# Kernel optimization log

Hardware: AMD Instinct MI355X
Metric: run time of the kernel (lower is better)

## Reference

```python
import jax, jax.numpy as jnp
import numpy as np

GRID_SIZE = 5
SPLINE_ORDER = 3
NUM_BASIS = GRID_SIZE + SPLINE_ORDER  # 8
BN_EPS = 1e-5


def make_grid():
    # efficient_kan extended uniform grid on [-1, 1]
    h = 2.0 / GRID_SIZE
    return (jnp.arange(-SPLINE_ORDER, GRID_SIZE + SPLINE_ORDER + 1, dtype=jnp.float32) * h) - 1.0


def b_splines(x, grid):
    """Cox-de Boor B-spline bases. x: (...,) -> (..., NUM_BASIS)."""
    x = x[..., None]
    bases = ((x >= grid[:-1]) & (x < grid[1:])).astype(x.dtype)
    for p in range(1, SPLINE_ORDER + 1):
        left = (x - grid[: -(p + 1)]) / (grid[p:-1] - grid[: -(p + 1)])
        right = (grid[p + 1:] - x) / (grid[p + 1:] - grid[1:-p])
        bases = left * bases[..., :-1] + right * bases[..., 1:]
    return bases


def grouped_conv(x, w, groups, padding):
    return jax.lax.conv_general_dilated(
        x, w, window_strides=(1, 1), padding=[(padding, padding)] * 2,
        feature_group_count=groups,
        dimension_numbers=("NCHW", "OIHW", "NCHW"))


def kan_conv(x, w_base, b_base, w_spline, grid, groups, padding):
    # base branch: grouped conv on SiLU(x)
    base = grouped_conv(jax.nn.silu(x), w_base, groups, padding)
    base = base + b_base[None, :, None, None]
    # spline branch: per-channel B-spline basis expansion (C -> C*NUM_BASIS)
    B, C, H, W = x.shape
    sp = b_splines(jnp.moveaxis(x, 1, -1), grid)            # (B,H,W,C,NB)
    sp = jnp.moveaxis(sp.reshape(B, H, W, C * NUM_BASIS), -1, 1)  # (B,C*NB,H,W)
    return base + grouped_conv(sp, w_spline, groups, padding)


def setup_inputs() -> dict:
    key = jax.random.key(0)
    ks = jax.random.split(key, 8)
    B, C_in, C_out, G, H, W = 16, 128, 256, 8, 64, 64
    x = jax.random.normal(ks[0], (B, C_in, H, W), dtype=jnp.float32)
    w_base1 = jax.random.normal(ks[1], (C_out, C_in // G, 1, 1), jnp.float32) * 0.1
    b_base1 = jnp.zeros((C_out,), jnp.float32)
    w_spline1 = jax.random.normal(ks[2], (C_out, (C_in * NUM_BASIS) // G, 1, 1), jnp.float32) * 0.05
    w_base2 = jax.random.normal(ks[3], (C_out, C_out // G, 3, 3), jnp.float32) * 0.05
    b_base2 = jnp.zeros((C_out,), jnp.float32)
    w_spline2 = jax.random.normal(ks[4], (C_out, (C_out * NUM_BASIS) // G, 3, 3), jnp.float32) * 0.02
    gamma = jnp.ones((C_out,), jnp.float32)
    beta = jnp.zeros((C_out,), jnp.float32)
    return {"x": x, "w_base1": w_base1, "b_base1": b_base1, "w_spline1": w_spline1,
            "w_base2": w_base2, "b_base2": b_base2, "w_spline2": w_spline2,
            "gamma": gamma, "beta": beta}


def reference(x, w_base1, b_base1, w_spline1, w_base2, b_base2, w_spline2, gamma, beta):
    G = 8
    grid = make_grid()
    h = kan_conv(x, w_base1, b_base1, w_spline1, grid, G, padding=0)   # 1x1 grouped KAN conv
    h = kan_conv(h, w_base2, b_base2, w_spline2, grid, G, padding=1)   # 3x3 grouped KAN conv
    # BatchNorm2d (training mode: batch statistics over N,H,W)
    mean = jnp.mean(h, axis=(0, 2, 3), keepdims=True)
    var = jnp.var(h, axis=(0, 2, 3), keepdims=True)
    hn = (h - mean) * jax.lax.rsqrt(var + BN_EPS)
    return hn * gamma[None, :, None, None] + beta[None, :, None, None]
```

## Files before the change

kernel.cpp:

```cpp
#include <hip/hip_runtime.h>
#include <hip/hip_bf16.h>
#include <stdint.h>


#define NB 8
#define NF 9
#define CIN 128
#define COUT 256
#define GROUPS 8
#define HW 4096
#define BATCH 16

#define WFS_ELEMS 589824
#define WFB_ELEMS 73728
#define WF1S_ELEMS 32768
#define WF1B_ELEMS 8192

typedef __attribute__((ext_vector_type(8))) short bf16x8;
typedef __attribute__((ext_vector_type(4))) float f32x4;

__device__ __forceinline__ unsigned bf16r(float f) {
    union { float f; unsigned u; } c; c.f = f;
    unsigned r = c.u + 0x7FFF + ((c.u >> 16) & 1);
    return r >> 16;
}
__device__ __forceinline__ unsigned bfpack2(float lo, float hi) {
    unsigned r;
    asm("v_cvt_pk_bf16_f32 %0, %1, %2" : "=v"(r) : "v"(lo), "v"(hi));
    return r;
}
__device__ __forceinline__ unsigned bfpack2_typed(float lo, float hi) {
    __hip_bfloat16 a = __float2bfloat16(lo);
    __hip_bfloat16 b = __float2bfloat16(hi);
    unsigned short ua, ub;
    __builtin_memcpy(&ua, &a, 2);
    __builtin_memcpy(&ub, &b, 2);
    return (unsigned)ua | ((unsigned)ub << 16);
}

__device__ __forceinline__ float silu_fast(float v) {
    float e = __builtin_amdgcn_exp2f(v * -1.44269504088896f);
    return v * __builtin_amdgcn_rcpf(1.0f + e);
}

__device__ __forceinline__ void spline_w(float v, float& w0, float& w1,
                                         float& w2, float& w3, int& k) {
    float s = (v + 2.2f) * 2.5f;
    float fk = floorf(s);
    k = (int)fk;
    float u = s - fk;
    float um = 1.0f - u;
    float u2 = u * u, u3 = u2 * u;
    w0 = um * um * um * (1.0f / 6.0f);
    w1 = (3.0f * u3 - 6.0f * u2 + 4.0f) * (1.0f / 6.0f);
    w2 = (-3.0f * u3 + 3.0f * u2 + 3.0f * u + 1.0f) * (1.0f / 6.0f);
    w3 = u3 * (1.0f / 6.0f);
}

__device__ __forceinline__ uint4 spline_row(float v, bool in, float& sv) {
    sv = silu_fast(v);
    float w0, w1, w2, w3; int k;
    spline_w(v, w0, w1, w2, w3, k);
    unsigned W0 = bfpack2(w0, w1);
    unsigned W1 = bfpack2(w2, w3);
    int kk = in ? (k - 3) : 99;
    unsigned odd = (unsigned)kk & 1u;
    unsigned A = W0 << 16;
    unsigned B = (W0 >> 16) | (W1 << 16);
    unsigned C = W1 >> 16;
    unsigned t0 = odd ? A : W0;
    unsigned t1 = odd ? B : W1;
    unsigned t2 = odd ? C : 0u;
    int q = kk >> 1;
    uint4 pk;
    pk.x = (q == 0) ? t0 : (q == -1) ? t1 : (q == -2) ? t2 : 0u;
    pk.y = (q == 1) ? t0 : (q == 0)  ? t1 : (q == -1) ? t2 : 0u;
    pk.z = (q == 2) ? t0 : (q == 1)  ? t1 : (q == 0)  ? t2 : 0u;
    pk.w = (q == 3) ? t0 : (q == 2)  ? t1 : (q == 1)  ? t2 : 0u;
    return pk;
}

__device__ __forceinline__ void expand_u(int raw, bool in,
                                         uint4& pk, unsigned& su) {
    float v = __uint_as_float(((unsigned)raw) << 16);
    float sv;
    pk = spline_row(v, in, sv);
    su = bf16r(sv);
}

__global__ void __launch_bounds__(256) repack2_kernel(
    const float* __restrict__ wb1, const float* __restrict__ ws1,
    const float* __restrict__ wb2, const float* __restrict__ ws2,
    unsigned short* __restrict__ wfs, unsigned short* __restrict__ wfb,
    unsigned short* __restrict__ wf1s, unsigned short* __restrict__ wf1b) {
    int i = blockIdx.x * 256 + threadIdx.x;
    if (i < WF1S_ELEMS) {
        int j = i & 7;
        int lane = (i >> 3) & 63;
        int nf = (i >> 9) & 1;
        int cc = (i >> 10) & 3;
        int g = i >> 12;
        int c_loc = cc * 4 + (lane >> 4);
        int cog = g * 32 + nf * 16 + (lane & 15);
        wf1s[i] = (unsigned short)bf16r(ws1[cog * 128 + c_loc * 8 + j]);
    }
    if (i < WF1B_ELEMS) {
        int j = i & 7;
        int lane = (i >> 3) & 63;
        int nf = (i >> 9) & 1;
        int g = (i >> 10) & 7;
        int k = (lane >> 4) * 8 + j;
        int cog = g * 32 + nf * 16 + (lane & 15);
        wf1b[i] = (k < 16) ? (unsigned short)bf16r(wb1[cog * 16 + k]) : 0;
    }
    if (i < WFB_ELEMS) {
        int j = i & 7;
        int lane = (i >> 3) & 63;
        int nf = (i >> 9) & 1;
        int t = i >> 10;
        int dy = t % 3; t /= 3;
        int dx = t % 3; t /= 3;
        int g = t;
        int ch = (lane >> 4) * 8 + j;
        int cog = g * 32 + nf * 16 + (lane & 15);
        wfb[i] = (unsigned short)bf16r(wb2[((cog * 32 + ch) * 3 + dy) * 3 + dx]);
    }
    if (i < WFS_ELEMS) {
        int j = i & 7;
        int t = i >> 3;
        int lane = t & 63; t >>= 6;
        int nf = t & 1; t >>= 1;
        int dy = t % 3; t /= 3;
        int dx = t % 3; t /= 3;
        int cc = t & 7; t >>= 3;
        int g = t;
        int c_loc = cc * 4 + (lane >> 4);
        int cog = g * 32 + nf * 16 + (lane & 15);
        float v = ws2[((cog * 256 + c_loc * 8 + j) * 3 + dy) * 3 + dx];
        wfs[i] = (unsigned short)bf16r(v);
    }
}

__global__ void __launch_bounds__(256, 4) kan1m_kernel(
    const float* __restrict__ x, const bf16x8* __restrict__ wf1s,
    const bf16x8* __restrict__ wf1b, const float* __restrict__ bb1,
    unsigned short* __restrict__ h1) {
    __shared__ __align__(16) unsigned char lds[32768];
    unsigned char* spl = lds;
    unsigned char* slu = lds + 16384;

    const int tid = threadIdx.x;
    const int lane = tid & 63;
    const int w = tid >> 6;
    const int blk = blockIdx.x;
    const int tile = blk & 15;
    const int g = (blk >> 4) & 7;
    const int b = blk >> 7;
    const int lrow = lane & 15;
    const int lhi = lane >> 4;
    const int posg0 = tile * 256;

    {
        int key = (tid >> 1) & 3;
        uint4 z = {0, 0, 0, 0};
        *reinterpret_cast<uint4*>(slu + tid * 64 + ((2 ^ key) << 4)) = z;
        *reinterpret_cast<uint4*>(slu + tid * 64 + ((3 ^ key) << 4)) = z;
    }

    const float* xg = x + ((size_t)b * CIN + g * 16) * HW + posg0;

    float xreg[4];
#pragma unroll
    for (int it = 0; it < 4; ++it) xreg[it] = xg[it * HW + tid];

    f32x4 acc[4][2];
#pragma unroll
    for (int m = 0; m < 4; ++m)
#pragma unroll
        for (int nf = 0; nf < 2; ++nf) {
            float bias = bb1[g * 32 + nf * 16 + lrow];
            acc[m][nf] = (f32x4){bias, bias, bias, bias};
        }

    for (int cc = 0; cc < 4; ++cc) {
        __syncthreads();
        int key = (tid >> 1) & 3;
#pragma unroll
        for (int it = 0; it < 4; ++it) {
            float sv;
            uint4 pk = spline_row(xreg[it], true, sv);
            *reinterpret_cast<uint4*>(spl + tid * 64 + ((it ^ key) << 4)) = pk;
            int cg = cc * 4 + it;
            *reinterpret_cast<unsigned short*>(
                slu + tid * 64 + (((cg >> 3) ^ key) << 4) + (cg & 7) * 2) =
                (unsigned short)bf16r(sv);
        }
        if (cc < 3) {
#pragma unroll
            for (int it = 0; it < 4; ++it)
                xreg[it] = xg[((cc + 1) * 4 + it) * HW + tid];
        }
        __syncthreads();
        const bf16x8* wpc = wf1s + (size_t)((g * 4 + cc) * 2) * 64;
        bf16x8 bf0 = wpc[lane];
        bf16x8 bf1 = wpc[64 + lane];
#pragma unroll
        for (int m = 0; m < 4; ++m) {
            int pos = w * 64 + m * 16 + lrow;
            int ra = pos * 64 + ((lhi ^ ((pos >> 1) & 3)) << 4);
            bf16x8 af = *reinterpret_cast<const bf16x8*>(spl + ra);
            acc[m][0] = __builtin_amdgcn_mfma_f32_16x16x32_bf16(af, bf0, acc[m][0], 0, 0, 0);
            acc[m][1] = __builtin_amdgcn_mfma_f32_16x16x32_bf16(af, bf1, acc[m][1], 0, 0, 0);
        }
    }
    {
        const bf16x8* wpb = wf1b + (size_t)(g * 2) * 64;
        bf16x8 bf0 = wpb[lane];
        bf16x8 bf1 = wpb[64 + lane];
#pragma unroll
        for (int m = 0; m < 4; ++m) {
            int pos = w * 64 + m * 16 + lrow;
            int ra = pos * 64 + ((lhi ^ ((pos >> 1) & 3)) << 4);
            bf16x8 af = *reinterpret_cast<const bf16x8*>(slu + ra);
            acc[m][0] = __builtin_amdgcn_mfma_f32_16x16x32_bf16(af, bf0, acc[m][0], 0, 0, 0);
            acc[m][1] = __builtin_amdgcn_mfma_f32_16x16x32_bf16(af, bf1, acc[m][1], 0, 0, 0);
        }
    }
#pragma unroll
    for (int m = 0; m < 4; ++m)
#pragma unroll
        for (int nf = 0; nf < 2; ++nf) {
            int co = g * 32 + nf * 16 + lrow;
            size_t base = ((size_t)b * COUT + co) * HW + posg0 + w * 64 + m * 16 + lhi * 4;
            uint2 o = {bfpack2_typed(acc[m][nf][0], acc[m][nf][1]),
                       bfpack2_typed(acc[m][nf][2], acc[m][nf][3])};
            *reinterpret_cast<uint2*>(&h1[base]) = o;
        }
}

__device__ __forceinline__ void mfma_hr(
    const unsigned char* __restrict__ base, const int (&ra)[6],
    const bf16x8 (&bf)[3][2], f32x4 (&acc)[4][2]) {
#pragma unroll
    for (int hr = 0; hr < 6; ++hr) {
        bf16x8 af = *reinterpret_cast<const bf16x8*>(base + ra[hr]);
#pragma unroll
        for (int dy = 0; dy < 3; ++dy) {
            int y = hr - dy;
            if (y >= 0 && y < 4) {
                acc[y][0] = __builtin_amdgcn_mfma_f32_16x16x32_bf16(af, bf[dy][0], acc[y][0], 0, 0, 0);
                acc[y][1] = __builtin_amdgcn_mfma_f32_16x16x32_bf16(af, bf[dy][1], acc[y][1], 0, 0, 0);
            }
        }
    }
}

__global__ void __launch_bounds__(256, 3) kan2_mfma5_kernel(
    const unsigned short* __restrict__ h1, const bf16x8* __restrict__ wfs,
    const bf16x8* __restrict__ wfb, const float* __restrict__ bb2,
    float* __restrict__ h2, float* __restrict__ partial2) {
    __shared__ __align__(16) unsigned char lds[41472];
    unsigned char* spl = lds;
    unsigned char* slu = lds + 20736;

    const int tid = threadIdx.x;
    const int lane = tid & 63;
    const int w = tid >> 6;
    const int blk = blockIdx.x;
    const int tile = blk & 15;
    const int g = (blk >> 4) & 7;
    const int b = blk >> 7;
    const int ty = (tile >> 2) * 16, tx = (tile & 3) * 16;
    const int lrow = lane & 15;
    const int lhi = lane >> 4;

    int offv[6], wadS[6], sluB[6], keysh[6];
#pragma unroll
    for (int it = 0; it < 6; ++it) {
        int e = tid + it * 256;
        int ch = (e * 3237) >> 20;
        int p = e - ch * 324;
        int hy = (p * 57) >> 10;
        int hx = p - hy * 18;
        int iy = ty + hy - 1, ix = tx + hx - 1;
        bool in = ((unsigned)iy < 64u) & ((unsigned)ix < 64u);
        offv[it] = in ? (ch * HW + iy * 64 + ix) : -1;
        int key = (p >> 1) & 3;
        wadS[it] = p * 64 + ((ch ^ key) << 4);
        sluB[it] = p * 64 + ch * 2;
        keysh[it] = key << 4;
    }

    const int pbase0 = (w * 4) * 18 + lrow;
    int raA[3][6];
#pragma unroll
    for (int dx = 0; dx < 3; ++dx)
#pragma unroll
        for (int hr = 0; hr < 6; ++hr) {
            int p = pbase0 + dx + hr * 18;
            raA[dx][hr] = p * 64 + ((lhi ^ ((p >> 1) & 3)) << 4);
        }

    const unsigned short* h1g = h1 + (size_t)(b * COUT + g * 32) * HW;

    int vregU[6];
    uint4 ereg[6];
    unsigned sreg[6];
#pragma unroll
    for (int it = 0; it < 6; ++it)
        if (it < 5 || tid < 16)
            vregU[it] = (offv[it] >= 0) ? (int)h1g[offv[it]] : 0;
#pragma unroll
    for (int it = 0; it < 6; ++it)
        if (it < 5 || tid < 16)
            expand_u(vregU[it], offv[it] >= 0, ereg[it], sreg[it]);
#pragma unroll
    for (int it = 0; it < 6; ++it)
        if (it < 5 || tid < 16)
            vregU[it] = (offv[it] >= 0) ? (int)h1g[4 * HW + offv[it]] : 0;

    f32x4 acc[4][2];
#pragma unroll
    for (int y = 0; y < 4; ++y)
#pragma unroll
        for (int nf = 0; nf < 2; ++nf) {
            float bias = bb2[g * 32 + nf * 16 + lrow];
            acc[y][nf] = (f32x4){bias, bias, bias, bias};
        }

    const bf16x8* wl = wfs + (size_t)(g * 8) * 18 * 64 + lane;

    for (int cc = 0; cc < 8; ++cc) {
        bf16x8 bf0[3][2];
#pragma unroll
        for (int dy = 0; dy < 3; ++dy)
#pragma unroll
            for (int nf = 0; nf < 2; ++nf)
                bf0[dy][nf] = wl[(dy * 2 + nf) * 64];

        __syncthreads();
        {
            int t4 = (cc >> 1) << 4;
            int u8 = (cc & 1) << 3;
#pragma unroll
            for (int it = 0; it < 6; ++it)
                if (it < 5 || tid < 16) {
                    *reinterpret_cast<uint4*>(spl + wadS[it]) = ereg[it];
                    *reinterpret_cast<unsigned short*>(
                        slu + sluB[it] + (t4 ^ keysh[it]) + u8) =
                        (unsigned short)sreg[it];
                }
        }
        __syncthreads();

        bf16x8 bf1[3][2], bf2[3][2];
#pragma unroll
        for (int dy = 0; dy < 3; ++dy)
#pragma unroll
            for (int nf = 0; nf < 2; ++nf)
                bf1[dy][nf] = wl[(6 + dy * 2 + nf) * 64];
        __builtin_amdgcn_s_setprio(1);
        mfma_hr(spl, raA[0], bf0, acc);
        __builtin_amdgcn_s_setprio(0);
#pragma unroll
        for (int dy = 0; dy < 3; ++dy)
#pragma unroll
            for (int nf = 0; nf < 2; ++nf)
                bf2[dy][nf] = wl[(12 + dy * 2 + nf) * 64];
        __builtin_amdgcn_s_setprio(1);
        mfma_hr(spl, raA[1], bf1, acc);
        __builtin_amdgcn_s_setprio(0);
        if (cc < 7) {
#pragma unroll
            for (int it = 0; it < 6; ++it)
                if (it < 5 || tid < 16)
                    expand_u(vregU[it], offv[it] >= 0, ereg[it], sreg[it]);
        }
        if (cc < 6) {
#pragma unroll
            for (int it = 0; it < 6; ++it)
                if (it < 5 || tid < 16)
                    vregU[it] = (offv[it] >= 0)
                        ? (int)h1g[(size_t)((cc + 2) * 4) * HW + offv[it]] : 0;
        }
        __builtin_amdgcn_s_setprio(1);
        mfma_hr(spl, raA[2], bf2, acc);
        __builtin_amdgcn_s_setprio(0);
        wl += 18 * 64;
    }

    {
        const bf16x8* wlb = wfb + (size_t)(g * 3) * 6 * 64 + lane;
#pragma unroll
        for (int dx = 0; dx < 3; ++dx) {
            bf16x8 bf[3][2];
#pragma unroll
            for (int dy = 0; dy < 3; ++dy)
#pragma unroll
                for (int nf = 0; nf < 2; ++nf)
                    bf[dy][nf] = wlb[(dx * 6 + dy * 2 + nf) * 64];
            __builtin_amdgcn_s_setprio(1);
            mfma_hr(slu, raA[dx], bf, acc);
            __builtin_amdgcn_s_setprio(0);
        }
    }

#pragma unroll
    for (int y = 0; y < 4; ++y) {
        int oy = ty + w * 4 + y;
#pragma unroll
        for (int nf = 0; nf < 2; ++nf) {
            int co = g * 32 + nf * 16 + lrow;
            float4 o = {acc[y][nf][0], acc[y][nf][1], acc[y][nf][2], acc[y][nf][3]};
            *reinterpret_cast<float4*>(
                &h2[(((size_t)b * COUT + co) * 64 + oy) * 64 + tx + lhi * 4]) = o;
        }
    }

    float s0 = 0.0f, q0 = 0.0f, s1 = 0.0f, q1 = 0.0f;
#pragma unroll
    for (int y = 0; y < 4; ++y)
#pragma unroll
        for (int i = 0; i < 4; ++i) {
            float a0 = acc[y][0][i], a1 = acc[y][1][i];
            s0 += a0; q0 = fmaf(a0, a0, q0);
            s1 += a1; q1 = fmaf(a1, a1, q1);
        }
    s0 += __shfl_xor(s0, 16); s0 += __shfl_xor(s0, 32);
    q0 += __shfl_xor(q0, 16); q0 += __shfl_xor(q0, 32);
    s1 += __shfl_xor(s1, 16); s1 += __shfl_xor(s1, 32);
    q1 += __shfl_xor(q1, 16); q1 += __shfl_xor(q1, 32);
    __syncthreads();
    float* stb = reinterpret_cast<float*>(lds);
    if (lane < 16) {
        int base = (w * 16 + lane) * 4;
        stb[base] = s0; stb[base + 1] = q0;
        stb[base + 2] = s1; stb[base + 3] = q1;
    }
    __syncthreads();
    if (tid < 64) {
        int slot = tid >> 1;
        int j = tid & 1;
        int lr = slot & 15, nf = slot >> 4;
        float a = 0.0f;
#pragma unroll
        for (int wv = 0; wv < 4; ++wv)
            a += stb[(wv * 16 + lr) * 4 + nf * 2 + j];
        partial2[blk * 64 + tid] = a;
    }
}

__global__ void __launch_bounds__(256) bnstat2_kernel(
    const float* __restrict__ partial2, const float* __restrict__ gamma,
    const float* __restrict__ beta, float* __restrict__ stats) {
    int co = blockIdx.x;
    int t = threadIdx.x;
    int g = co >> 5, loc = co & 31;
    int b = t >> 4, tile = t & 15;
    int blk = (b * 8 + g) * 16 + tile;
    float s = partial2[blk * 64 + loc * 2];
    float ss = partial2[blk * 64 + loc * 2 + 1];
    __shared__ float r1[256], r2[256];
    r1[t] = s; r2[t] = ss;
    __syncthreads();
    for (int o = 128; o > 0; o >>= 1) {
        if (t < o) { r1[t] += r1[t + o]; r2[t] += r2[t + o]; }
        __syncthreads();
    }
    if (t == 0) {
        const float invn = 1.0f / 65536.0f;
        float mean = r1[0] * invn;
        float var = r2[0] * invn - mean * mean;
        float sc = gamma[co] * rsqrtf(var + 1e-5f);
        stats[2 * co] = sc;
        stats[2 * co + 1] = beta[co] - mean * sc;
    }
}

__global__ void __launch_bounds__(256) bnapply_kernel(
    float* __restrict__ h2, const float* __restrict__ stats, int n4) {
    int i = blockIdx.x * 256 + threadIdx.x;
    if (i >= n4) return;
    int co = (i >> 10) & 255;
    float sc = stats[2 * co], sh = stats[2 * co + 1];
    float4 v = reinterpret_cast<float4*>(h2)[i];
    float4 o;
    o.x = fmaf(v.x, sc, sh);
    o.y = fmaf(v.y, sc, sh);
    o.z = fmaf(v.z, sc, sh);
    o.w = fmaf(v.w, sc, sh);
    reinterpret_cast<float4*>(h2)[i] = o;
}

extern "C" void kernel_launch(void* const* d_in, const int* in_sizes, int n_in,
                              void* d_out, int out_size, void* d_ws, size_t ws_size,
                              hipStream_t stream) {
    const float* x   = (const float*)d_in[0];
    const float* wb1 = (const float*)d_in[1];
    const float* bb1 = (const float*)d_in[2];
    const float* ws1 = (const float*)d_in[3];
    const float* wb2 = (const float*)d_in[4];
    const float* bb2 = (const float*)d_in[5];
    const float* ws2 = (const float*)d_in[6];
    const float* gamma = (const float*)d_in[7];
    const float* beta  = (const float*)d_in[8];

    char* ws = (char*)d_ws;
    unsigned short* wfs  = (unsigned short*)ws;
    unsigned short* wfb  = (unsigned short*)(ws + 1179648);
    unsigned short* wf1s = (unsigned short*)(ws + 1327104);
    unsigned short* wf1b = (unsigned short*)(ws + 1392640);
    float* partial2 = (float*)(ws + 1409024);
    float* stats    = (float*)(ws + 1933312);
    unsigned short* h1 = (unsigned short*)(ws + 1935360);

    float* h2 = (float*)d_out;

    repack2_kernel<<<(WFS_ELEMS + 255) / 256, 256, 0, stream>>>(
        wb1, ws1, wb2, ws2, wfs, wfb, wf1s, wf1b);
    kan1m_kernel<<<BATCH * GROUPS * 16, 256, 0, stream>>>(
        x, (const bf16x8*)wf1s, (const bf16x8*)wf1b, bb1, h1);
    kan2_mfma5_kernel<<<BATCH * GROUPS * 16, 256, 0, stream>>>(
        h1, (const bf16x8*)wfs, (const bf16x8*)wfb, bb2, h2, partial2);
    bnstat2_kernel<<<COUT, 256, 0, stream>>>(partial2, gamma, beta, stats);
    bnapply_kernel<<<(4194304 + 255) / 256, 256, 0, stream>>>(
        h2, stats, 4194304);
}
```

Before: 150.1 us.

## Double-buffer spline LDS tiles and store pre-BN output as bf16

The 3x3 KAN conv kernel now alternates between two LDS buffers for the spline tile, which removes one __syncthreads per channel-chunk iteration. LDS use grows to about 62 KB, so the occupancy hint drops from 3 to 2 blocks. The pre-BN activation is written to workspace as bf16 rather than fp32, and the BN apply kernel reads bf16 and writes fp32 output, cutting intermediate memory traffic. In exchange, the output loses precision because it is rounded to bf16 before normalisation, and fewer blocks can run per CU.

Result: slower. 153.8 us (+2.4%).

```diff
diff --git a/kernel.cpp b/kernel.cpp
--- a/kernel.cpp
+++ b/kernel.cpp
@@ -255,13 +255,14 @@
     }
 }
 
-__global__ void __launch_bounds__(256, 3) kan2_mfma5_kernel(
+__global__ void __launch_bounds__(256, 2) kan2_db_kernel(
     const unsigned short* __restrict__ h1, const bf16x8* __restrict__ wfs,
     const bf16x8* __restrict__ wfb, const float* __restrict__ bb2,
-    float* __restrict__ h2, float* __restrict__ partial2) {
-    __shared__ __align__(16) unsigned char lds[41472];
-    unsigned char* spl = lds;
-    unsigned char* slu = lds + 20736;
+    unsigned short* __restrict__ hb, float* __restrict__ partial2) {
+    __shared__ __align__(16) unsigned char lds[62208];
+    unsigned char* spl0 = lds;
+    unsigned char* spl1 = lds + 20736;
+    unsigned char* slu  = lds + 41472;
 
     const int tid = threadIdx.x;
     const int lane = tid & 63;
@@ -331,6 +332,7 @@
     const bf16x8* wl = wfs + (size_t)(g * 8) * 18 * 64 + lane;
 
     for (int cc = 0; cc < 8; ++cc) {
+        unsigned char* bufR = (cc & 1) ? spl1 : spl0;
         bf16x8 bf0[3][2];
 #pragma unroll
         for (int dy = 0; dy < 3; ++dy)
@@ -338,14 +340,13 @@
             for (int nf = 0; nf < 2; ++nf)
                 bf0[dy][nf] = wl[(dy * 2 + nf) * 64];
 
-        __syncthreads();
         {
             int t4 = (cc >> 1) << 4;
             int u8 = (cc & 1) << 3;
 #pragma unroll
             for (int it = 0; it < 6; ++it)
                 if (it < 5 || tid < 16) {
-                    *reinterpret_cast<uint4*>(spl + wadS[it]) = ereg[it];
+                    *reinterpret_cast<uint4*>(bufR + wadS[it]) = ereg[it];
                     *reinterpret_cast<unsigned short*>(
                         slu + sluB[it] + (t4 ^ keysh[it]) + u8) =
                         (unsigned short)sreg[it];
@@ -360,7 +361,7 @@
             for (int nf = 0; nf < 2; ++nf)
                 bf1[dy][nf] = wl[(6 + dy * 2 + nf) * 64];
         __builtin_amdgcn_s_setprio(1);
-        mfma_hr(spl, raA[0], bf0, acc);
+        mfma_hr(bufR, raA[0], bf0, acc);
         __builtin_amdgcn_s_setprio(0);
 #pragma unroll
         for (int dy = 0; dy < 3; ++dy)
@@ -368,7 +369,7 @@
             for (int nf = 0; nf < 2; ++nf)
                 bf2[dy][nf] = wl[(12 + dy * 2 + nf) * 64];
         __builtin_amdgcn_s_setprio(1);
-        mfma_hr(spl, raA[1], bf1, acc);
+        mfma_hr(bufR, raA[1], bf1, acc);
         __builtin_amdgcn_s_setprio(0);
         if (cc < 7) {
 #pragma unroll
@@ -384,10 +385,11 @@
                         ? (int)h1g[(size_t)((cc + 2) * 4) * HW + offv[it]] : 0;
         }
         __builtin_amdgcn_s_setprio(1);
-        mfma_hr(spl, raA[2], bf2, acc);
+        mfma_hr(bufR, raA[2], bf2, acc);
         __builtin_amdgcn_s_setprio(0);
         wl += 18 * 64;
     }
+    __syncthreads();
 
     {
         const bf16x8* wlb = wfb + (size_t)(g * 3) * 6 * 64 + lane;
@@ -411,9 +413,10 @@
 #pragma unroll
         for (int nf = 0; nf < 2; ++nf) {
             int co = g * 32 + nf * 16 + lrow;
-            float4 o = {acc[y][nf][0], acc[y][nf][1], acc[y][nf][2], acc[y][nf][3]};
-            *reinterpret_cast<float4*>(
-                &h2[(((size_t)b * COUT + co) * 64 + oy) * 64 + tx + lhi * 4]) = o;
+            uint2 o = {bfpack2_typed(acc[y][nf][0], acc[y][nf][1]),
+                       bfpack2_typed(acc[y][nf][2], acc[y][nf][3])};
+            *reinterpret_cast<uint2*>(
+                &hb[(((size_t)b * COUT + co) * 64 + oy) * 64 + tx + lhi * 4]) = o;
         }
     }
 
@@ -478,18 +481,24 @@
 }
 
 __global__ void __launch_bounds__(256) bnapply_kernel(
-    float* __restrict__ h2, const float* __restrict__ stats, int n4) {
+    const unsigned short* __restrict__ hb, const float* __restrict__ stats,
+    float* __restrict__ out) {
     int i = blockIdx.x * 256 + threadIdx.x;
-    if (i >= n4) return;
-    int co = (i >> 10) & 255;
+    int co = (i >> 9) & 255;
     float sc = stats[2 * co], sh = stats[2 * co + 1];
-    float4 v = reinterpret_cast<float4*>(h2)[i];
-    float4 o;
-    o.x = fmaf(v.x, sc, sh);
-    o.y = fmaf(v.y, sc, sh);
-    o.z = fmaf(v.z, sc, sh);
-    o.w = fmaf(v.w, sc, sh);
-    reinterpret_cast<float4*>(h2)[i] = o;
+    uint4 v = *reinterpret_cast<const uint4*>(hb + (size_t)i * 8);
+    float4 o0, o1;
+    o0.x = fmaf(__uint_as_float(v.x << 16), sc, sh);
+    o0.y = fmaf(__uint_as_float(v.x & 0xFFFF0000u), sc, sh);
+    o0.z = fmaf(__uint_as_float(v.y << 16), sc, sh);
+    o0.w = fmaf(__uint_as_float(v.y & 0xFFFF0000u), sc, sh);
+    o1.x = fmaf(__uint_as_float(v.z << 16), sc, sh);
+    o1.y = fmaf(__uint_as_float(v.z & 0xFFFF0000u), sc, sh);
+    o1.z = fmaf(__uint_as_float(v.w << 16), sc, sh);
+    o1.w = fmaf(__uint_as_float(v.w & 0xFFFF0000u), sc, sh);
+    float4* op = reinterpret_cast<float4*>(out + (size_t)i * 8);
+    op[0] = o0;
+    op[1] = o1;
 }
 
 extern "C" void kernel_launch(void* const* d_in, const int* in_sizes, int n_in,
@@ -513,16 +522,14 @@
     float* partial2 = (float*)(ws + 1409024);
     float* stats    = (float*)(ws + 1933312);
     unsigned short* h1 = (unsigned short*)(ws + 1935360);
-
-    float* h2 = (float*)d_out;
+    unsigned short* hb = (unsigned short*)(ws + 35489792);
 
     repack2_kernel<<<(WFS_ELEMS + 255) / 256, 256, 0, stream>>>(
         wb1, ws1, wb2, ws2, wfs, wfb, wf1s, wf1b);
     kan1m_kernel<<<BATCH * GROUPS * 16, 256, 0, stream>>>(
         x, (const bf16x8*)wf1s, (const bf16x8*)wf1b, bb1, h1);
-    kan2_mfma5_kernel<<<BATCH * GROUPS * 16, 256, 0, stream>>>(
-        h1, (const bf16x8*)wfs, (const bf16x8*)wfb, bb2, h2, partial2);
+    kan2_db_kernel<<<BATCH * GROUPS * 16, 256, 0, stream>>>(
+        h1, (const bf16x8*)wfs, (const bf16x8*)wfb, bb2, hb, partial2);
     bnstat2_kernel<<<COUT, 256, 0, stream>>>(partial2, gamma, beta, stats);
-    bnapply_kernel<<<(4194304 + 255) / 256, 256, 0, stream>>>(
-        h2, stats, 4194304);
-}
+    bnapply_kernel<<<8192, 256, 0, stream>>>(hb, stats, (float*)d_out);
+}
```
